# Performance work log

Measured on AMD Instinct MI355X. Metric: run time of the kernel, lower is better.

## Reference

```python
import jax, jax.numpy as jnp
import numpy as np

E, B, L, H1, H2, C = 8, 4096, 512, 1024, 512, 40


def setup_inputs() -> dict:
    key = jax.random.key(0)
    ks = jax.random.split(key, 9)
    return {
        "x_s": jax.random.normal(ks[0], (B, L), jnp.float32),
        "x_p": jax.random.normal(ks[1], (B, L), jnp.float32),
        "W1": jax.random.normal(ks[2], (E, 2 * L, H1), jnp.float32) / np.sqrt(2 * L).astype(np.float32),
        "b1": jax.random.normal(ks[3], (E, H1), jnp.float32) * 0.01,
        "W2": jax.random.normal(ks[4], (E, H1, H2), jnp.float32) / np.sqrt(H1).astype(np.float32),
        "b2": jax.random.normal(ks[5], (E, H2), jnp.float32) * 0.01,
        "W3": jax.random.normal(ks[6], (E, H2, C), jnp.float32) / np.sqrt(H2).astype(np.float32),
        "b3": jax.random.normal(ks[7], (E, C), jnp.float32) * 0.01,
        "sub_module_label": jax.random.randint(ks[8], (B,), 0, E, dtype=jnp.int32),
        "sub_id": 0,
    }


def reference(x_s, x_p, W1, b1, W2, b2, W3, b3, sub_module_label, sub_id):
    # Encoders (EEGNet/SCN/DCN) abstracted as identity: x_s / x_p are latent features.
    # Cls_HEAD.forward: x = cat([x_p, x_s], dim=1); per-sample routed 3-layer ELU MLP head.
    # Dropout is identity in eval mode.
    x = jnp.concatenate([x_p, x_s], axis=1)                      # [B, 2L]
    h = jax.nn.elu(jnp.einsum('bi,eih->ebh', x, W1) + b1[:, None, :])   # [E, B, H1]
    h = jax.nn.elu(jnp.einsum('ebh,ehk->ebk', h, W2) + b2[:, None, :])  # [E, B, H2]
    out_all = jnp.einsum('ebk,ekc->ebc', h, W3) + b3[:, None, :]        # [E, B, C]
    # select each sample's routed expert output
    bidx = jnp.arange(x.shape[0])
    return out_all[sub_module_label, bidx]                       # [B, C]
```

## Files before the change

kernel.cpp:

```cpp
#include <hip/hip_runtime.h>
#include <hip/hip_bf16.h>
#include <math.h>

#define En   8
#define Bn   4096
#define Ln   512
#define K1n  1024
#define H1n  1024
#define H2n  512
#define Cn   40
#define NP3  48

typedef unsigned short u16;
typedef __attribute__((ext_vector_type(8))) short bf16x8;
typedef __attribute__((ext_vector_type(4))) float f32x4;

__device__ __forceinline__ u16 f2b(float f) {
    union { float f; unsigned int u; } v; v.f = f;
    unsigned int r = v.u + 0x7FFF + ((v.u >> 16) & 1);
    return (u16)(r >> 16);
}

__device__ __forceinline__ void g2l16(const void* g, void* l) {
    __builtin_amdgcn_global_load_lds(
        (const __attribute__((address_space(1))) unsigned int*)(unsigned long long)g,
        (__attribute__((address_space(3))) unsigned int*)(unsigned int)(unsigned long long)l,
        16, 0, 0);
}

#define PB_X0   1
#define PB_X    256
#define PB_W1   2048
#define PB_W2   1024
#define PB_W3   128
#define PB_OUT  64
#define PB_TOT  (PB_X0 + PB_X + PB_W1 + PB_W2 + PB_W3 + PB_OUT)

__device__ __forceinline__ void wtrans64(
    const float* __restrict__ Wsrc, u16* __restrict__ Wdst,
    int K, int N, int k0, int n0, int tid, float* sm )
{
    #pragma unroll
    for (int s = 0; s < 4; s++) {
        int idx = tid + s * 256;
        int kk = idx >> 4, c4 = (idx & 15) * 4;
        float4 v = *(const float4*)&Wsrc[(size_t)(k0 + kk) * N + n0 + c4];
        float* row = sm + kk * 65 + c4;
        row[0] = v.x; row[1] = v.y; row[2] = v.z; row[3] = v.w;
    }
    __syncthreads();
    #pragma unroll
    for (int s = 0; s < 4; s++) {
        int idx = tid + s * 256;
        int nn = idx >> 4, kc = (idx & 15) * 4;
        ushort4 o = make_ushort4(f2b(sm[(kc + 0) * 65 + nn]), f2b(sm[(kc + 1) * 65 + nn]),
                                 f2b(sm[(kc + 2) * 65 + nn]), f2b(sm[(kc + 3) * 65 + nn]));
        *(ushort4*)&Wdst[(size_t)(n0 + nn) * K + k0 + kc] = o;
    }
}

__global__ __launch_bounds__(256) void prep_kernel(
    const float* __restrict__ xs, const float* __restrict__ xp,
    const float* __restrict__ W1, const float* __restrict__ W2,
    const float* __restrict__ W3, const float* __restrict__ b3,
    const int* __restrict__ label,
    int* __restrict__ meta, int* __restrict__ perm,
    u16* __restrict__ Xb, u16* __restrict__ W1t,
    u16* __restrict__ W2t, u16* __restrict__ W3t,
    float* __restrict__ out)
{
    __shared__ __align__(16) float sm[64 * 65];
    const int bid = blockIdx.x;
    const int tid = threadIdx.x;

    if (bid == 0) {
        int* cnt = (int*)sm;
        int* off = cnt + En;
        if (tid < En) cnt[tid] = 0;
        __syncthreads();
        for (int b = tid; b < Bn; b += 256) atomicAdd(&cnt[label[b]], 1);
        __syncthreads();
        if (tid == 0) {
            int run = 0;
            for (int e = 0; e < En; e++) { off[e] = run; run += cnt[e]; }
            off[En] = run;
        }
        __syncthreads();
        if (tid < En) cnt[tid] = off[tid];
        __syncthreads();
        for (int b = tid; b < Bn; b += 256) {
            int e = label[b];
            perm[atomicAdd(&cnt[e], 1)] = b;
        }
        if (tid <= En) meta[tid] = off[tid];
    } else if (bid < PB_X0 + PB_X) {
        int r0 = (bid - PB_X0) * 16;
        #pragma unroll 4
        for (int s = 0; s < 16; s++) {
            int r = r0 + s;
            int k = tid * 4;
            const float* src = (k < Ln) ? (xp + (size_t)r * Ln + k)
                                        : (xs + (size_t)r * Ln + (k - Ln));
            float4 v = *(const float4*)src;
            *(ushort4*)&Xb[(size_t)r * K1n + k] =
                make_ushort4(f2b(v.x), f2b(v.y), f2b(v.z), f2b(v.w));
        }
    } else if (bid < PB_X0 + PB_X + PB_W1) {
        int b = bid - (PB_X0 + PB_X);
        int e = b >> 8, rem = b & 255;
        int k0 = (rem >> 4) * 64, n0 = (rem & 15) * 64;
        wtrans64(W1 + (size_t)e * K1n * H1n, W1t + (size_t)e * H1n * K1n,
                 K1n, H1n, k0, n0, tid, sm);
    } else if (bid < PB_X0 + PB_X + PB_W1 + PB_W2) {
        int b = bid - (PB_X0 + PB_X + PB_W1);
        int e = b >> 7, rem = b & 127;
        int k0 = (rem >> 3) * 64, n0 = (rem & 7) * 64;
        wtrans64(W2 + (size_t)e * H1n * H2n, W2t + (size_t)e * H2n * H1n,
                 H1n, H2n, k0, n0, tid, sm);
    } else if (bid < PB_X0 + PB_X + PB_W1 + PB_W2 + PB_W3) {
        int b = bid - (PB_X0 + PB_X + PB_W1 + PB_W2);
        int e = b >> 4, k0 = (b & 15) * 32;
        const float* src = W3 + (size_t)e * H2n * Cn;
        u16* dst = W3t + (size_t)e * NP3 * H2n;
        float* t = sm;
        #pragma unroll
        for (int s = 0; s < 5; s++) {
            int idx = tid + s * 256;
            int kk = idx / Cn, nn = idx - kk * Cn;
            if (kk < 32) t[kk * 41 + nn] = src[(size_t)(k0 + kk) * Cn + nn];
        }
        __syncthreads();
        #pragma unroll
        for (int s = 0; s < 6; s++) {
            int idx = tid + s * 256;
            int nn = idx >> 5, kk = idx & 31;
            float v = (nn < Cn) ? t[kk * 41 + nn] : 0.f;
            dst[(size_t)nn * H2n + k0 + kk] = f2b(v);
        }
    } else {
        int b = bid - (PB_X0 + PB_X + PB_W1 + PB_W2 + PB_W3);
        int r0 = b * 64;
        #pragma unroll
        for (int s = 0; s < 10; s++) {
            int idx = tid + s * 256;
            int r = r0 + idx / Cn;
            int c = idx - (idx / Cn) * Cn;
            out[(size_t)r * Cn + c] = b3[label[r] * Cn + c];
        }
    }
}

template <int K, int N, bool GATHER, bool FUSE3>
__global__ __launch_bounds__(256) void mfma_gemm(
    const u16* __restrict__ A, const u16* __restrict__ Wt,
    const float* __restrict__ bias, const int* __restrict__ meta,
    const int* __restrict__ perm, u16* __restrict__ outb,
    const u16* __restrict__ Wt3, float* __restrict__ outf)
{
    constexpr int TM = 128, TN = 128, BK = 64;
    constexpr int T = K / BK;
    __shared__ __align__(16) u16 SM[32768];

    const int tid = threadIdx.x;
    const int bx = blockIdx.x;

    int expert = -1, row0 = 0, rowmax = 0, acc_t = 0;
    int prev = meta[0];
    #pragma unroll
    for (int e = 0; e < En; e++) {
        int nxt = meta[e + 1];
        int c = nxt - prev;
        int t = (c + TM - 1) / TM;
        if (expert < 0 && bx < acc_t + t) {
            expert = e; row0 = prev + (bx - acc_t) * TM; rowmax = nxt - 1;
        }
        acc_t += t; prev = nxt;
    }
    if (expert < 0) return;

    const int col0 = blockIdx.y * TN;
    const u16* Wexp = Wt + (size_t)expert * N * K;

    const int lane = tid & 63;
    const int wid = tid >> 6;
    const int wm = (wid & 1) * 64;
    const int wn = (wid >> 1) * 64;
    const int l15 = lane & 15;
    const int lq = lane >> 4;

    const u16* aptr[4]; const u16* bptr[4];
    int aoff[4], boff[4];
    #pragma unroll
    for (int s = 0; s < 4; s++) {
        int idx = tid + s * 256;
        int rl = idx >> 3, c = idx & 7;
        int kq = c ^ (rl & 7);
        int rg = row0 + rl; if (rg > rowmax) rg = rowmax;
        if (GATHER) rg = perm[rg];
        aptr[s] = A + (size_t)rg * K + kq * 8;
        bptr[s] = Wexp + (size_t)(col0 + rl) * K + kq * 8;
        aoff[s] = idx * 8;
        boff[s] = 8192 + idx * 8;
    }
    const int csw = l15 & 7;

    f32x4 acc[4][4];
    #pragma unroll
    for (int i = 0; i < 4; i++)
        #pragma unroll
        for (int j = 0; j < 4; j++) acc[i][j] = (f32x4){0.f, 0.f, 0.f, 0.f};

    #pragma unroll
    for (int s = 0; s < 4; s++) {
        g2l16(aptr[s], &SM[aoff[s]]);
        g2l16(bptr[s], &SM[boff[s]]);
    }

    for (int t = 0; t < T; t++) {
        __syncthreads();
        const u16* As = &SM[(t & 1) * 16384];
        const u16* Bs = As + 8192;
        if (t + 1 < T) {
            int base = ((t + 1) & 1) * 16384;
            int ko = (t + 1) * BK;
            #pragma unroll
            for (int s = 0; s < 4; s++) {
                g2l16(aptr[s] + ko, &SM[base + aoff[s]]);
                g2l16(bptr[s] + ko, &SM[base + boff[s]]);
            }
        }
        bf16x8 af[4][2], bf[4][2];
        #pragma unroll
        for (int h = 0; h < 2; h++) {
            const int ksw = (((h * 4 + lq) ^ csw)) * 8;
            #pragma unroll
            for (int i = 0; i < 4; i++)
                af[i][h] = *(const bf16x8*)&As[(wm + i * 16 + l15) * BK + ksw];
            #pragma unroll
            for (int j = 0; j < 4; j++)
                bf[j][h] = *(const bf16x8*)&Bs[(wn + j * 16 + l15) * BK + ksw];
        }
        #pragma unroll
        for (int h = 0; h < 2; h++)
            #pragma unroll
            for (int i = 0; i < 4; i++)
                #pragma unroll
                for (int j = 0; j < 4; j++)
                    acc[i][j] = __builtin_amdgcn_mfma_f32_16x16x32_bf16(
                        af[i][h], bf[j][h], acc[i][j], 0, 0, 0);
    }

    if (!FUSE3) {
        #pragma unroll
        for (int i = 0; i < 4; i++) {
            #pragma unroll
            for (int j = 0; j < 4; j++) {
                int col = col0 + wn + j * 16 + l15;
                float bv = bias[expert * N + col];
                #pragma unroll
                for (int r = 0; r < 4; r++) {
                    int grow = row0 + wm + i * 16 + lq * 4 + r;
                    if (grow <= rowmax) {
                        float v = acc[i][j][r] + bv;
                        v = (v > 0.f) ? v : (expf(v) - 1.f);
                        outb[(size_t)grow * N + col] = f2b(v);
                    }
                }
            }
        }
    } else {
        __syncthreads();
        u16* H = &SM[0];
        #pragma unroll
        for (int i = 0; i < 4; i++) {
            #pragma unroll
            for (int j = 0; j < 4; j++) {
                int col = wn + j * 16 + l15;
                float bv = bias[expert * N + col0 + col];
                #pragma unroll
                for (int r = 0; r < 4; r++) {
                    float v = acc[i][j][r] + bv;
                    v = (v > 0.f) ? v : (expf(v) - 1.f);
                    H[(wm + i * 16 + lq * 4 + r) * 136 + col] = f2b(v);
                }
            }
        }
        __syncthreads();
        const int rh = (wid & 1) * 64;
        const int kb = (wid >> 1) * 64;
        f32x4 a3[4][3];
        #pragma unroll
        for (int i = 0; i < 4; i++)
            #pragma unroll
            for (int j = 0; j < 3; j++) a3[i][j] = (f32x4){0.f, 0.f, 0.f, 0.f};
        #pragma unroll
        for (int ki = 0; ki < 2; ki++) {
            int kl = kb + ki * 32;
            bf16x8 ha[4];
            #pragma unroll
            for (int i = 0; i < 4; i++)
                ha[i] = *(const bf16x8*)&H[(rh + i * 16 + l15) * 136 + kl + lq * 8];
            #pragma unroll
            for (int j = 0; j < 3; j++) {
                bf16x8 wb = *(const bf16x8*)
                    &Wt3[((size_t)expert * NP3 + j * 16 + l15) * H2n + col0 + kl + lq * 8];
                #pragma unroll
                for (int i = 0; i < 4; i++)
                    a3[i][j] = __builtin_amdgcn_mfma_f32_16x16x32_bf16(
                        ha[i], wb, a3[i][j], 0, 0, 0);
            }
        }
        #pragma unroll
        for (int j = 0; j < 3; j++) {
            int col = j * 16 + l15;
            if (col < Cn) {
                #pragma unroll
                for (int i = 0; i < 4; i++) {
                    #pragma unroll
                    for (int r = 0; r < 4; r++) {
                        int grow = row0 + rh + i * 16 + lq * 4 + r;
                        if (grow <= rowmax)
                            atomicAdd(&outf[(size_t)perm[grow] * Cn + col], a3[i][j][r]);
                    }
                }
            }
        }
    }
}

extern "C" void kernel_launch(void* const* d_in, const int* in_sizes, int n_in,
                              void* d_out, int out_size, void* d_ws, size_t ws_size,
                              hipStream_t stream)
{
    const float* xs = (const float*)d_in[0];
    const float* xp = (const float*)d_in[1];
    const float* W1 = (const float*)d_in[2];
    const float* b1 = (const float*)d_in[3];
    const float* W2 = (const float*)d_in[4];
    const float* b2 = (const float*)d_in[5];
    const float* W3 = (const float*)d_in[6];
    const float* b3 = (const float*)d_in[7];
    const int* label = (const int*)d_in[8];
    float* out = (float*)d_out;

    char* ws = (char*)d_ws;
    int* meta = (int*)ws;
    int* perm = (int*)(ws + 64);
    u16* Xb  = (u16*)(ws + (64 << 10));
    u16* W1t = (u16*)(ws + (64 << 10) + (8  << 20));
    u16* W2t = (u16*)(ws + (64 << 10) + (24 << 20));
    u16* h1b = (u16*)(ws + (64 << 10) + (32 << 20));
    u16* W3t = (u16*)(ws + (64 << 10) + (40 << 20));

    prep_kernel<<<PB_TOT, 256, 0, stream>>>(
        xs, xp, W1, W2, W3, b3, label, meta, perm, Xb, W1t, W2t, W3t, out);

    mfma_gemm<K1n, H1n, true, false><<<dim3(40, 8), 256, 0, stream>>>(
        Xb, W1t, b1, meta, perm, h1b, nullptr, nullptr);

    mfma_gemm<H1n, H2n, false, true><<<dim3(40, 4), 256, 0, stream>>>(
        h1b, W2t, b2, meta, perm, nullptr, W3t, out);
}
```

Before: 180.9 us.

## Fuse W1/W2 fp32-to-bf16 transpose into GEMM B-tile loads

Removes the separate prep-kernel pass that transposed and converted W1 and W2 to bf16 in a workspace. The GEMMs now read the fp32 weights directly into registers, prefetched one K-step ahead, and convert and transpose them into swizzled LDS during the main loop. This avoids writing and re-reading about 24 MB of bf16 weights. In exchange, each tile re-reads and re-converts fp32 weights (twice the bytes per load, repeated across row tiles), uses more registers, and adds ALU work inside the loop.

```diff
diff --git a/kernel.cpp b/kernel.cpp
--- a/kernel.cpp
+++ b/kernel.cpp
@@ -30,52 +30,24 @@
 
 #define PB_X0   1
 #define PB_X    256
-#define PB_W1   2048
-#define PB_W2   1024
 #define PB_W3   128
 #define PB_OUT  64
-#define PB_TOT  (PB_X0 + PB_X + PB_W1 + PB_W2 + PB_W3 + PB_OUT)
-
-__device__ __forceinline__ void wtrans64(
-    const float* __restrict__ Wsrc, u16* __restrict__ Wdst,
-    int K, int N, int k0, int n0, int tid, float* sm )
-{
-    #pragma unroll
-    for (int s = 0; s < 4; s++) {
-        int idx = tid + s * 256;
-        int kk = idx >> 4, c4 = (idx & 15) * 4;
-        float4 v = *(const float4*)&Wsrc[(size_t)(k0 + kk) * N + n0 + c4];
-        float* row = sm + kk * 65 + c4;
-        row[0] = v.x; row[1] = v.y; row[2] = v.z; row[3] = v.w;
-    }
-    __syncthreads();
-    #pragma unroll
-    for (int s = 0; s < 4; s++) {
-        int idx = tid + s * 256;
-        int nn = idx >> 4, kc = (idx & 15) * 4;
-        ushort4 o = make_ushort4(f2b(sm[(kc + 0) * 65 + nn]), f2b(sm[(kc + 1) * 65 + nn]),
-                                 f2b(sm[(kc + 2) * 65 + nn]), f2b(sm[(kc + 3) * 65 + nn]));
-        *(ushort4*)&Wdst[(size_t)(n0 + nn) * K + k0 + kc] = o;
-    }
-}
+#define PB_TOT  (PB_X0 + PB_X + PB_W3 + PB_OUT)
 
 __global__ __launch_bounds__(256) void prep_kernel(
     const float* __restrict__ xs, const float* __restrict__ xp,
-    const float* __restrict__ W1, const float* __restrict__ W2,
     const float* __restrict__ W3, const float* __restrict__ b3,
     const int* __restrict__ label,
     int* __restrict__ meta, int* __restrict__ perm,
-    u16* __restrict__ Xb, u16* __restrict__ W1t,
-    u16* __restrict__ W2t, u16* __restrict__ W3t,
+    u16* __restrict__ Xb, u16* __restrict__ W3t,
     float* __restrict__ out)
 {
-    __shared__ __align__(16) float sm[64 * 65];
+    __shared__ __align__(16) float sm[32 * 41];
     const int bid = blockIdx.x;
     const int tid = threadIdx.x;
 
     if (bid == 0) {
-        int* cnt = (int*)sm;
-        int* off = cnt + En;
+        __shared__ int cnt[En], off[En + 1];
         if (tid < En) cnt[tid] = 0;
         __syncthreads();
         for (int b = tid; b < Bn; b += 256) atomicAdd(&cnt[label[b]], 1);
@@ -105,40 +77,27 @@
             *(ushort4*)&Xb[(size_t)r * K1n + k] =
                 make_ushort4(f2b(v.x), f2b(v.y), f2b(v.z), f2b(v.w));
         }
-    } else if (bid < PB_X0 + PB_X + PB_W1) {
+    } else if (bid < PB_X0 + PB_X + PB_W3) {
         int b = bid - (PB_X0 + PB_X);
-        int e = b >> 8, rem = b & 255;
-        int k0 = (rem >> 4) * 64, n0 = (rem & 15) * 64;
-        wtrans64(W1 + (size_t)e * K1n * H1n, W1t + (size_t)e * H1n * K1n,
-                 K1n, H1n, k0, n0, tid, sm);
-    } else if (bid < PB_X0 + PB_X + PB_W1 + PB_W2) {
-        int b = bid - (PB_X0 + PB_X + PB_W1);
-        int e = b >> 7, rem = b & 127;
-        int k0 = (rem >> 3) * 64, n0 = (rem & 7) * 64;
-        wtrans64(W2 + (size_t)e * H1n * H2n, W2t + (size_t)e * H2n * H1n,
-                 H1n, H2n, k0, n0, tid, sm);
-    } else if (bid < PB_X0 + PB_X + PB_W1 + PB_W2 + PB_W3) {
-        int b = bid - (PB_X0 + PB_X + PB_W1 + PB_W2);
         int e = b >> 4, k0 = (b & 15) * 32;
         const float* src = W3 + (size_t)e * H2n * Cn;
         u16* dst = W3t + (size_t)e * NP3 * H2n;
-        float* t = sm;
         #pragma unroll
         for (int s = 0; s < 5; s++) {
             int idx = tid + s * 256;
             int kk = idx / Cn, nn = idx - kk * Cn;
-            if (kk < 32) t[kk * 41 + nn] = src[(size_t)(k0 + kk) * Cn + nn];
+            if (kk < 32) sm[kk * 41 + nn] = src[(size_t)(k0 + kk) * Cn + nn];
         }
         __syncthreads();
         #pragma unroll
         for (int s = 0; s < 6; s++) {
             int idx = tid + s * 256;
             int nn = idx >> 5, kk = idx & 31;
-            float v = (nn < Cn) ? t[kk * 41 + nn] : 0.f;
+            float v = (nn < Cn) ? sm[kk * 41 + nn] : 0.f;
             dst[(size_t)nn * H2n + k0 + kk] = f2b(v);
         }
     } else {
-        int b = bid - (PB_X0 + PB_X + PB_W1 + PB_W2 + PB_W3);
+        int b = bid - (PB_X0 + PB_X + PB_W3);
         int r0 = b * 64;
         #pragma unroll
         for (int s = 0; s < 10; s++) {
@@ -150,9 +109,30 @@
     }
 }
 
+__device__ __forceinline__ void bstore(
+    const float4 wreg[2][4], u16* __restrict__ Bst, int kg, int n4)
+{
+    #pragma unroll
+    for (int p = 0; p < 2; p++) {
+        int k0 = (kg + p * 8) * 4;
+        float4 a0 = wreg[p][0], a1 = wreg[p][1], a2 = wreg[p][2], a3 = wreg[p][3];
+        ushort4 o[4];
+        o[0] = make_ushort4(f2b(a0.x), f2b(a1.x), f2b(a2.x), f2b(a3.x));
+        o[1] = make_ushort4(f2b(a0.y), f2b(a1.y), f2b(a2.y), f2b(a3.y));
+        o[2] = make_ushort4(f2b(a0.z), f2b(a1.z), f2b(a2.z), f2b(a3.z));
+        o[3] = make_ushort4(f2b(a0.w), f2b(a1.w), f2b(a2.w), f2b(a3.w));
+        #pragma unroll
+        for (int i = 0; i < 4; i++) {
+            int n = n4 + i;
+            int sig = (n ^ (n >> 2)) & 7;
+            *(ushort4*)&Bst[n * 64 + (k0 ^ (sig << 3))] = o[i];
+        }
+    }
+}
+
 template <int K, int N, bool GATHER, bool FUSE3>
 __global__ __launch_bounds__(256) void mfma_gemm(
-    const u16* __restrict__ A, const u16* __restrict__ Wt,
+    const u16* __restrict__ A, const float* __restrict__ Wf,
     const float* __restrict__ bias, const int* __restrict__ meta,
     const int* __restrict__ perm, u16* __restrict__ outb,
     const u16* __restrict__ Wt3, float* __restrict__ outf)
@@ -179,7 +159,7 @@
     if (expert < 0) return;
 
     const int col0 = blockIdx.y * TN;
-    const u16* Wexp = Wt + (size_t)expert * N * K;
+    const float* Wexp = Wf + (size_t)expert * K * N;
 
     const int lane = tid & 63;
     const int wid = tid >> 6;
@@ -188,8 +168,8 @@
     const int l15 = lane & 15;
     const int lq = lane >> 4;
 
-    const u16* aptr[4]; const u16* bptr[4];
-    int aoff[4], boff[4];
+    const u16* aptr[4];
+    int aoff[4];
     #pragma unroll
     for (int s = 0; s < 4; s++) {
         int idx = tid + s * 256;
@@ -198,23 +178,35 @@
         int rg = row0 + rl; if (rg > rowmax) rg = rowmax;
         if (GATHER) rg = perm[rg];
         aptr[s] = A + (size_t)rg * K + kq * 8;
-        bptr[s] = Wexp + (size_t)(col0 + rl) * K + kq * 8;
         aoff[s] = idx * 8;
-        boff[s] = 8192 + idx * 8;
     }
     const int csw = l15 & 7;
 
+    const int n4 = (tid & 31) * 4;
+    const int kg = tid >> 5;
+
+    int sB[4];
+    #pragma unroll
+    for (int j = 0; j < 4; j++) {
+        int n = wn + j * 16 + l15;
+        sB[j] = (n ^ (n >> 2)) & 7;
+    }
+
     f32x4 acc[4][4];
     #pragma unroll
     for (int i = 0; i < 4; i++)
         #pragma unroll
         for (int j = 0; j < 4; j++) acc[i][j] = (f32x4){0.f, 0.f, 0.f, 0.f};
 
-    #pragma unroll
-    for (int s = 0; s < 4; s++) {
-        g2l16(aptr[s], &SM[aoff[s]]);
-        g2l16(bptr[s], &SM[boff[s]]);
-    }
+    float4 wreg[2][4];
+    #pragma unroll
+    for (int p = 0; p < 2; p++)
+        #pragma unroll
+        for (int d = 0; d < 4; d++)
+            wreg[p][d] = *(const float4*)&Wexp[(size_t)((kg + p * 8) * 4 + d) * N + col0 + n4];
+    #pragma unroll
+    for (int s = 0; s < 4; s++) g2l16(aptr[s], &SM[aoff[s]]);
+    bstore(wreg, &SM[8192], kg, n4);
 
     for (int t = 0; t < T; t++) {
         __syncthreads();
@@ -224,21 +216,26 @@
             int base = ((t + 1) & 1) * 16384;
             int ko = (t + 1) * BK;
             #pragma unroll
-            for (int s = 0; s < 4; s++) {
+            for (int s = 0; s < 4; s++)
                 g2l16(aptr[s] + ko, &SM[base + aoff[s]]);
-                g2l16(bptr[s] + ko, &SM[base + boff[s]]);
-            }
+            #pragma unroll
+            for (int p = 0; p < 2; p++)
+                #pragma unroll
+                for (int d = 0; d < 4; d++)
+                    wreg[p][d] = *(const float4*)
+                        &Wexp[(size_t)(ko + (kg + p * 8) * 4 + d) * N + col0 + n4];
         }
         bf16x8 af[4][2], bf[4][2];
         #pragma unroll
         for (int h = 0; h < 2; h++) {
-            const int ksw = (((h * 4 + lq) ^ csw)) * 8;
             #pragma unroll
             for (int i = 0; i < 4; i++)
-                af[i][h] = *(const bf16x8*)&As[(wm + i * 16 + l15) * BK + ksw];
+                af[i][h] = *(const bf16x8*)
+                    &As[(wm + i * 16 + l15) * 64 + (((h * 4 + lq) ^ csw) << 3)];
             #pragma unroll
             for (int j = 0; j < 4; j++)
-                bf[j][h] = *(const bf16x8*)&Bs[(wn + j * 16 + l15) * BK + ksw];
+                bf[j][h] = *(const bf16x8*)
+                    &Bs[(wn + j * 16 + l15) * 64 + (((h * 4 + lq) ^ sB[j]) << 3)];
         }
         #pragma unroll
         for (int h = 0; h < 2; h++)
@@ -248,6 +245,8 @@
                 for (int j = 0; j < 4; j++)
                     acc[i][j] = __builtin_amdgcn_mfma_f32_16x16x32_bf16(
                         af[i][h], bf[j][h], acc[i][j], 0, 0, 0);
+        if (t + 1 < T)
+            bstore(wreg, &SM[((t + 1) & 1) * 16384 + 8192], kg, n4);
     }
 
     if (!FUSE3) {
@@ -347,17 +346,15 @@
     int* meta = (int*)ws;
     int* perm = (int*)(ws + 64);
     u16* Xb  = (u16*)(ws + (64 << 10));
-    u16* W1t = (u16*)(ws + (64 << 10) + (8  << 20));
-    u16* W2t = (u16*)(ws + (64 << 10) + (24 << 20));
-    u16* h1b = (u16*)(ws + (64 << 10) + (32 << 20));
-    u16* W3t = (u16*)(ws + (64 << 10) + (40 << 20));
+    u16* h1b = (u16*)(ws + (64 << 10) + (8 << 20));
+    u16* W3t = (u16*)(ws + (64 << 10) + (16 << 20));
 
     prep_kernel<<<PB_TOT, 256, 0, stream>>>(
-        xs, xp, W1, W2, W3, b3, label, meta, perm, Xb, W1t, W2t, W3t, out);
+        xs, xp, W3, b3, label, meta, perm, Xb, W3t, out);
 
     mfma_gemm<K1n, H1n, true, false><<<dim3(40, 8), 256, 0, stream>>>(
-        Xb, W1t, b1, meta, perm, h1b, nullptr, nullptr);
+        Xb, W1, b1, meta, perm, h1b, nullptr, nullptr);
 
     mfma_gemm<H1n, H2n, false, true><<<dim3(40, 4), 256, 0, stream>>>(
-        h1b, W2t, b2, meta, perm, nullptr, W3t, out);
-}
+        h1b, W2, b2, meta, perm, nullptr, W3t, out);
+}
```

Measured after the change: 200.1 us. 1.11x slower.
